# Optimization experiments

Measured on AMD Instinct MI355X. Metric: run time of the kernel, lower is better.

## Reference

```python
import jax, jax.numpy as jnp
import numpy as np
import math

B, H, W = 32, 512, 512
BS = 8
QUALITY = 50.0  # __scale_quality(75) = 200 - 2*75


def _make_dctmtx(bs=BS):
    m = np.empty((bs, bs), dtype=np.float32)
    for j in range(bs):
        for i in range(bs):
            if i == 0:
                m[i, j] = 1.0 / math.sqrt(bs)
            else:
                m[i, j] = math.sqrt(2.0 / bs) * math.cos(math.pi * (2 * j + 1) * i / (2 * bs))
    return jnp.asarray(m)


def _make_quantize():
    qY = np.array([[16,11,10,16,24,40,51,61],[12,12,14,19,26,58,60,55],
                   [14,13,16,24,40,57,69,56],[14,17,22,29,51,87,80,62],
                   [18,22,37,56,68,109,103,77],[24,35,55,64,81,104,113,92],
                   [49,64,78,87,103,121,120,101],[72,92,95,98,112,100,103,99]], dtype=np.float32) / 255.0
    qC = np.array([[17,18,24,47,99,99,99,99],[18,21,26,66,99,99,99,99],
                   [24,26,56,99,99,99,99,99],[47,66,99,99,99,99,99,99],
                   [99,99,99,99,99,99,99,99],[99,99,99,99,99,99,99,99],
                   [99,99,99,99,99,99,99,99],[99,99,99,99,99,99,99,99]], dtype=np.float32) / 255.0
    return jnp.asarray(np.stack([qY, qC, qC], axis=0))


def setup_inputs() -> dict:
    key = jax.random.key(0)
    x = jax.random.uniform(key, (B, 3, H, W), dtype=jnp.float32)
    return {"input": x, "quantize": _make_quantize(), "dctmtx": _make_dctmtx()}


def reference(input, quantize, dctmtx):
    bs = BS
    b, c, h, w = input.shape
    dt = input.dtype
    rgb = 255.0 * input
    # rgb -> ycbcr (3x3 color transform, offset cb/cr by 128, clamp)
    xf = jnp.array([[0.299, 0.587, 0.114],
                    [-0.168735892, -0.331264108, 0.5],
                    [0.5, -0.418687589, -0.081312411]], dtype=dt)
    off = jnp.array([0.0, 128.0, 128.0], dtype=dt)[None, :, None, None]
    ycbcr = jnp.clip(jnp.einsum('bchw,kc->bkhw', rgb, xf) + off, 0.0, 255.0)
    # 2x2 chroma subsample: replace Cb/Cr by 2x2 block means (Y untouched)
    yc = ycbcr[:, :1]
    cc = ycbcr[:, 1:].reshape(b, 2, h // 2, 2, w // 2, 2)
    cm = jnp.mean(cc, axis=(3, 5), keepdims=True)
    cc = jnp.broadcast_to(cm, cc.shape).reshape(b, 2, h, w)
    sample = jnp.concatenate([yc, cc], axis=1) - 128.0
    # extract 8x8 blocks -> [b, h/bs, w/bs, 3, bs, bs]
    blocks = sample.reshape(b, 3, h // bs, bs, w // bs, bs).transpose(0, 2, 4, 1, 3, 5)
    # 2D DCT: D @ X @ D^T
    dcts = jnp.einsum('ij,bhwcjk,lk->bhwcil', dctmtx, blocks, dctmtx)
    # quality-scaled quant table (broadcasts [3,8,8] over blocks)
    q = jnp.round(jnp.clip(jnp.round((jnp.round(quantize * 255.0) * QUALITY + 50.0) / 100.0), 1.0, 255.0))
    comp = jnp.round(dcts / q)
    decomp = jnp.round(comp * jax.lax.stop_gradient(q))
    # IDCT: D^T @ X @ D
    idcts = jnp.einsum('ji,bhwcjk,kl->bhwcil', dctmtx, decomp, dctmtx)
    # merge blocks back -> [b,3,h,w]
    ycbcr2 = idcts.transpose(0, 3, 1, 4, 2, 5).reshape(b, 3, h, w) + 128.0
    # ycbcr -> rgb
    xf2 = jnp.array([[1.0, 0.0, 1.402],
                     [1.0, -0.344136286, -0.714136286],
                     [1.0, 1.772, 0.0]], dtype=dt)
    im = ycbcr2 - off
    rgb2 = jnp.clip(jnp.einsum('bchw,kc->bkhw', im, xf2), 0.0, 255.0)
    return jnp.round(rgb2) / 255.0
```

## Files before the change

### kernel.cpp

```cpp
#include <hip/hip_runtime.h>

#define IN_H 512
#define IN_W 512


__device__ __forceinline__ float dpp_xor1(float x) {
    return __int_as_float(__builtin_amdgcn_mov_dpp(__float_as_int(x), 0xB1, 0xF, 0xF, true));
}
__device__ __forceinline__ float dpp_xor2(float x) {
    return __int_as_float(__builtin_amdgcn_mov_dpp(__float_as_int(x), 0x4E, 0xF, 0xF, true));
}
__device__ __forceinline__ float dpp_xor4(float x) {
    int i = __builtin_amdgcn_mov_dpp(__float_as_int(x), 0x141, 0xF, 0xF, true);
    i     = __builtin_amdgcn_mov_dpp(i,                 0x1B,  0xF, 0xF, true);
    return __int_as_float(i);
}

__global__ __launch_bounds__(256, 2) void jpeg_kernel(
    const float* __restrict__ in, const float* __restrict__ qz,
    const float* __restrict__ dmtx, float* __restrict__ out)
{
    __shared__ __align__(16) unsigned char smem[30464];
    double*  Ys  = (double*) (smem);
    double*  CbS = (double*) (smem + 17408);
    double*  CrS = (double*) (smem + 22016);
    double2* qt  = (double2*)(smem + 26624);
    double*  Dd  = (double*) (smem + 30080);
    float*   Dh  = (float*)  (smem + 30336);

    const int t   = threadIdx.x;
    const int blk = blockIdx.x;
    const int b   = blk >> 7;
    const int rr  = blk & 127;
    const int row0 = (rr >> 1) << 3;
    const int col0 = (rr & 1) << 8;
    const int chs = IN_H * IN_W;

    const int tile = t >> 3;
    const int h4   = (t >> 2) & 1;
    const int s    = t & 3;

    const int base = ((b * 3) * IN_H + row0 + 2 * s) * IN_W + col0 + tile * 8 + 4 * h4;
    float4 ra = *(const float4*)(in + base);
    float4 rb = *(const float4*)(in + base + IN_W);
    float4 ga = *(const float4*)(in + base + chs);
    float4 gb = *(const float4*)(in + base + chs + IN_W);
    float4 ba = *(const float4*)(in + base + 2 * chs);
    float4 bb = *(const float4*)(in + base + 2 * chs + IN_W);

    if (t < 192) {
        const int c = t >> 6, i = (t >> 3) & 7, l = t & 7;
        double v  = (double)qz[t];
        double t1 = rint((rint(v * 255.0) * 50.0 + 50.0) / 100.0);
        double q  = fmin(fmax(t1, 1.0), 255.0);
        qt[(c * 8 + l) * 9 + i] = make_double2(1.0 / q, q);
    }
    if (t < 32) {
        float dv = dmtx[(t >> 2) * 8 + (t & 3)];
        Dd[t] = (double)dv;
        Dh[t] = dv;
    }
    __syncthreads();

    {
        float rA[2][4] = {{ra.x,ra.y,ra.z,ra.w},{rb.x,rb.y,rb.z,rb.w}};
        float gA[2][4] = {{ga.x,ga.y,ga.z,ga.w},{gb.x,gb.y,gb.z,gb.w}};
        float bA[2][4] = {{ba.x,ba.y,ba.z,ba.w},{bb.x,bb.y,bb.z,bb.w}};

        double yv[2][4], cbv[2][4], crv[2][4];
        #pragma unroll
        for (int p = 0; p < 2; ++p) {
            #pragma unroll
            for (int k = 0; k < 4; ++k) {
                double R = 255.0 * (double)rA[p][k];
                double G = 255.0 * (double)gA[p][k];
                double B = 255.0 * (double)bA[p][k];
                double y  =  0.299*R + 0.587*G + 0.114*B;
                double cb = -0.168735892*R - 0.331264108*G + 0.5*B + 128.0;
                double cr =  0.5*R - 0.418687589*G - 0.081312411*B + 128.0;
                yv[p][k]  = fmin(fmax(y , 0.0), 255.0) - 128.0;
                cbv[p][k] = fmin(fmax(cb, 0.0), 255.0);
                crv[p][k] = fmin(fmax(cr, 0.0), 255.0);
            }
        }
        #pragma unroll
        for (int p = 0; p < 2; ++p) {
            double* yp = &Ys[tile * 68 + (2*s + p) * 8 + 4 * h4];
            *(double2*)(yp)     = make_double2(yv[p][0], yv[p][1]);
            *(double2*)(yp + 2) = make_double2(yv[p][2], yv[p][3]);
        }
        double m0 = (cbv[0][0]+cbv[0][1]+cbv[1][0]+cbv[1][1])*0.25 - 128.0;
        double m1 = (cbv[0][2]+cbv[0][3]+cbv[1][2]+cbv[1][3])*0.25 - 128.0;
        *(double2*)&CbS[tile * 18 + s * 4 + 2 * h4] = make_double2(m0, m1);
        double n0 = (crv[0][0]+crv[0][1]+crv[1][0]+crv[1][1])*0.25 - 128.0;
        double n1 = (crv[0][2]+crv[0][3]+crv[1][2]+crv[1][3])*0.25 - 128.0;
        *(double2*)&CrS[tile * 18 + s * 4 + 2 * h4] = make_double2(n0, n1);
    }
    __builtin_amdgcn_wave_barrier();

    const int q8 = t >> 3;
    const int l  = t & 7;
    double dl0, dl1, dl2, dl3;
    {
        double2 dA = *(const double2*)&Dd[l * 4];
        double2 dB = *(const double2*)&Dd[l * 4 + 2];
        dl0 = dA.x; dl1 = dA.y; dl2 = dB.x; dl3 = dB.y;
    }
    const double sgn  = (l & 1) ? -1.0 : 1.0;
    const double dl01 = dl0 + dl1, dl23 = dl2 + dl3;
    const bool sel1 = (l & 1) != 0;
    const bool sel2 = (l & 2) != 0;
    const bool sel4 = (l & 4) != 0;

    double e20[4], o20[4];
    {
        const double* basep = &Ys[q8 * 68];
        #pragma unroll
        for (int m = 0; m < 4; ++m) {
            double tp[2];
            #pragma unroll
            for (int hh = 0; hh < 2; ++hh) {
                const double* p = basep + (hh ? (7 - m) : m) * 8;
                double2 a0 = *(const double2*)(p);
                double2 a1 = *(const double2*)(p + 2);
                double2 a2 = *(const double2*)(p + 4);
                double2 a3 = *(const double2*)(p + 6);
                double v0 = fma(sgn, a3.y, a0.x);
                double v1 = fma(sgn, a3.x, a0.y);
                double v2 = fma(sgn, a2.y, a1.x);
                double v3 = fma(sgn, a2.x, a1.y);
                tp[hh] = dl0*v0 + dl1*v1 + dl2*v2 + dl3*v3;
            }
            e20[m] = tp[0] + tp[1];
            o20[m] = tp[0] - tp[1];
        }
    }
    double e21[4], o21[4], e22[4], o22[4];
    #pragma unroll
    for (int cc = 0; cc < 2; ++cc) {
        const double* basep = (cc == 0 ? CbS : CrS) + q8 * 18;
        double u4[4];
        #pragma unroll
        for (int j2 = 0; j2 < 4; ++j2) {
            double2 a0 = *(const double2*)(basep + j2 * 4);
            double2 a1 = *(const double2*)(basep + j2 * 4 + 2);
            u4[j2] = dl01 * fma(sgn, a1.y, a0.x) + dl23 * fma(sgn, a1.x, a0.y);
        }
        double ea = u4[0] + u4[3], oa = u4[0] - u4[3];
        double eb = u4[1] + u4[2], ob = u4[1] - u4[2];
        if (cc == 0) { e21[0]=e21[1]=ea; o21[0]=o21[1]=oa; e21[2]=e21[3]=eb; o21[2]=o21[3]=ob; }
        else         { e22[0]=e22[1]=ea; o22[0]=o22[1]=oa; e22[2]=e22[3]=eb; o22[2]=o22[3]=ob; }
    }

    float zo[3][8];
    {
        const double2* dd2 = (const double2*)Dd;
        #pragma unroll
        for (int i = 0; i < 8; ++i) {
            double2 dA = dd2[i * 2], dB = dd2[i * 2 + 1];
            #define ZQ(C, E, O) { \
                double a64 = (i & 1) \
                    ? dA.x*O[0] + dA.y*O[1] + dB.x*O[2] + dB.y*O[3] \
                    : dA.x*E[0] + dA.y*E[1] + dB.x*E[2] + dB.y*E[3]; \
                double2 qe = qt[(C * 8 + l) * 9 + i]; \
                zo[C][i] = (float)(rint(a64 * qe.x) * qe.y); }
            ZQ(0, e20, o20)
            ZQ(1, e21, o21)
            ZQ(2, e22, o22)
            #undef ZQ
        }
    }

    const float4* dh4p = (const float4*)Dh;
    float4 d0 = dh4p[0], d1 = dh4p[1], d2 = dh4p[2], d3 = dh4p[3];
    float4 d4 = dh4p[4], d5 = dh4p[5], d6 = dh4p[6], d7 = dh4p[7];

    float acc[3][8];

    #define BFLY(XF, SS, A, B) { float _t = (SS) ? (A) : (B); float _tx = XF(_t); \
                                 (A) = (SS) ? _tx : (A); (B) = (SS) ? (B) : _tx; }

    #define EPI(C) { \
        float se0 = zo[C][0]*d0.x + zo[C][2]*d2.x + zo[C][4]*d4.x + zo[C][6]*d6.x; \
        float se1 = zo[C][0]*d0.y + zo[C][2]*d2.y + zo[C][4]*d4.y + zo[C][6]*d6.y; \
        float se2 = zo[C][0]*d0.z + zo[C][2]*d2.z + zo[C][4]*d4.z + zo[C][6]*d6.z; \
        float se3 = zo[C][0]*d0.w + zo[C][2]*d2.w + zo[C][4]*d4.w + zo[C][6]*d6.w; \
        float so0 = zo[C][1]*d1.x + zo[C][3]*d3.x + zo[C][5]*d5.x + zo[C][7]*d7.x; \
        float so1 = zo[C][1]*d1.y + zo[C][3]*d3.y + zo[C][5]*d5.y + zo[C][7]*d7.y; \
        float so2 = zo[C][1]*d1.z + zo[C][3]*d3.z + zo[C][5]*d5.z + zo[C][7]*d7.z; \
        float so3 = zo[C][1]*d1.w + zo[C][3]*d3.w + zo[C][5]*d5.w + zo[C][7]*d7.w; \
        float u0 = se0+so0, u7 = se0-so0; \
        float u1 = se1+so1, u6 = se1-so1; \
        float u2 = se2+so2, u5 = se2-so2; \
        float u3 = se3+so3, u4v = se3-so3; \
         \
        BFLY(dpp_xor1, sel1, u0, u1)  BFLY(dpp_xor1, sel1, u2, u3) \
        BFLY(dpp_xor1, sel1, u4v, u5) BFLY(dpp_xor1, sel1, u6, u7) \
        BFLY(dpp_xor2, sel2, u0, u2)  BFLY(dpp_xor2, sel2, u1, u3) \
        BFLY(dpp_xor2, sel2, u4v, u6) BFLY(dpp_xor2, sel2, u5, u7) \
        BFLY(dpp_xor4, sel4, u0, u4v) BFLY(dpp_xor4, sel4, u1, u5) \
        BFLY(dpp_xor4, sel4, u2, u6)  BFLY(dpp_xor4, sel4, u3, u7) \
        float re0 = u0*d0.x + u2*d2.x + u4v*d4.x + u6*d6.x; \
        float re1 = u0*d0.y + u2*d2.y + u4v*d4.y + u6*d6.y; \
        float re2 = u0*d0.z + u2*d2.z + u4v*d4.z + u6*d6.z; \
        float re3 = u0*d0.w + u2*d2.w + u4v*d4.w + u6*d6.w; \
        float ro0 = u1*d1.x + u3*d3.x + u5*d5.x + u7*d7.x; \
        float ro1 = u1*d1.y + u3*d3.y + u5*d5.y + u7*d7.y; \
        float ro2 = u1*d1.z + u3*d3.z + u5*d5.z + u7*d7.z; \
        float ro3 = u1*d1.w + u3*d3.w + u5*d5.w + u7*d7.w; \
        acc[C][0]=re0+ro0; acc[C][7]=re0-ro0; \
        acc[C][1]=re1+ro1; acc[C][6]=re1-ro1; \
        acc[C][2]=re2+ro2; acc[C][5]=re2-ro2; \
        acc[C][3]=re3+ro3; acc[C][4]=re3-ro3; }

    EPI(0)
    EPI(1)
    EPI(2)
    #undef EPI
    #undef BFLY

    {
        const int obase = ((b * 3) * IN_H + row0 + l) * IN_W + col0 + q8 * 8;
        float R4[8], G4[8], B4[8];
        #pragma unroll
        for (int y = 0; y < 8; ++y) {
            float im0 = acc[0][y] + 128.0f;
            float im1 = acc[1][y];
            float im2 = acc[2][y];
            float R  = fminf(fmaxf(im0 + 1.402f*im2, 0.0f), 255.0f);
            float G  = fminf(fmaxf(im0 - 0.344136286f*im1 - 0.714136286f*im2, 0.0f), 255.0f);
            float Bv = fminf(fmaxf(im0 + 1.772f*im1, 0.0f), 255.0f);
            R4[y] = rintf(R)  * (1.0f/255.0f);
            G4[y] = rintf(G)  * (1.0f/255.0f);
            B4[y] = rintf(Bv) * (1.0f/255.0f);
        }
        *(float4*)(out + obase)               = make_float4(R4[0],R4[1],R4[2],R4[3]);
        *(float4*)(out + obase + 4)           = make_float4(R4[4],R4[5],R4[6],R4[7]);
        *(float4*)(out + obase + chs)         = make_float4(G4[0],G4[1],G4[2],G4[3]);
        *(float4*)(out + obase + chs + 4)     = make_float4(G4[4],G4[5],G4[6],G4[7]);
        *(float4*)(out + obase + 2*chs)       = make_float4(B4[0],B4[1],B4[2],B4[3]);
        *(float4*)(out + obase + 2*chs + 4)   = make_float4(B4[4],B4[5],B4[6],B4[7]);
    }
}

extern "C" void kernel_launch(void* const* d_in, const int* in_sizes, int n_in,
                              void* d_out, int out_size, void* d_ws, size_t ws_size,
                              hipStream_t stream) {
    (void)in_sizes; (void)n_in; (void)out_size; (void)d_ws; (void)ws_size;
    const float* in  = (const float*)d_in[0];
    const float* qz  = (const float*)d_in[1];
    const float* dm  = (const float*)d_in[2];
    float* out = (float*)d_out;
    dim3 grid(4096), blk(256);
    hipLaunchKernelGGL(jpeg_kernel, grid, blk, 0, stream, in, qz, dm, out);
}
```

Before: 182.2 us.

## Compute luma row DCT in registers via DPP exchanges instead of shared memory

```diff
diff --git a/kernel.cpp b/kernel.cpp
--- a/kernel.cpp
+++ b/kernel.cpp
@@ -16,17 +16,37 @@
     return __int_as_float(i);
 }
 
+__device__ __forceinline__ double dpp_xor1_d(double x) {
+    union { double d; int i[2]; } u; u.d = x;
+    u.i[0] = __builtin_amdgcn_mov_dpp(u.i[0], 0xB1, 0xF, 0xF, true);
+    u.i[1] = __builtin_amdgcn_mov_dpp(u.i[1], 0xB1, 0xF, 0xF, true);
+    return u.d;
+}
+__device__ __forceinline__ double dpp_xor2_d(double x) {
+    union { double d; int i[2]; } u; u.d = x;
+    u.i[0] = __builtin_amdgcn_mov_dpp(u.i[0], 0x4E, 0xF, 0xF, true);
+    u.i[1] = __builtin_amdgcn_mov_dpp(u.i[1], 0x4E, 0xF, 0xF, true);
+    return u.d;
+}
+__device__ __forceinline__ double dpp_xor4_d(double x) {
+    union { double d; int i[2]; } u; u.d = x;
+    u.i[0] = __builtin_amdgcn_mov_dpp(u.i[0], 0x141, 0xF, 0xF, true);
+    u.i[0] = __builtin_amdgcn_mov_dpp(u.i[0], 0x1B,  0xF, 0xF, true);
+    u.i[1] = __builtin_amdgcn_mov_dpp(u.i[1], 0x141, 0xF, 0xF, true);
+    u.i[1] = __builtin_amdgcn_mov_dpp(u.i[1], 0x1B,  0xF, 0xF, true);
+    return u.d;
+}
+
 __global__ __launch_bounds__(256, 2) void jpeg_kernel(
     const float* __restrict__ in, const float* __restrict__ qz,
     const float* __restrict__ dmtx, float* __restrict__ out)
 {
-    __shared__ __align__(16) unsigned char smem[30464];
-    double*  Ys  = (double*) (smem);
-    double*  CbS = (double*) (smem + 17408);
-    double*  CrS = (double*) (smem + 22016);
-    double2* qt  = (double2*)(smem + 26624);
-    double*  Dd  = (double*) (smem + 30080);
-    float*   Dh  = (float*)  (smem + 30336);
+    __shared__ __align__(16) unsigned char smem[13056];
+    double*  CbS = (double*) (smem);
+    double*  CrS = (double*) (smem + 4608);
+    double2* qt  = (double2*)(smem + 9216);
+    double*  Dd  = (double*) (smem + 12672);
+    float*   Dh  = (float*)  (smem + 12928);
 
     const int t   = threadIdx.x;
     const int blk = blockIdx.x;
@@ -62,12 +82,13 @@
     }
     __syncthreads();
 
+    double yv[2][4];
     {
         float rA[2][4] = {{ra.x,ra.y,ra.z,ra.w},{rb.x,rb.y,rb.z,rb.w}};
         float gA[2][4] = {{ga.x,ga.y,ga.z,ga.w},{gb.x,gb.y,gb.z,gb.w}};
         float bA[2][4] = {{ba.x,ba.y,ba.z,ba.w},{bb.x,bb.y,bb.z,bb.w}};
 
-        double yv[2][4], cbv[2][4], crv[2][4];
+        double cbv[2][4], crv[2][4];
         #pragma unroll
         for (int p = 0; p < 2; ++p) {
             #pragma unroll
@@ -83,12 +104,6 @@
                 crv[p][k] = fmin(fmax(cr, 0.0), 255.0);
             }
         }
-        #pragma unroll
-        for (int p = 0; p < 2; ++p) {
-            double* yp = &Ys[tile * 68 + (2*s + p) * 8 + 4 * h4];
-            *(double2*)(yp)     = make_double2(yv[p][0], yv[p][1]);
-            *(double2*)(yp + 2) = make_double2(yv[p][2], yv[p][3]);
-        }
         double m0 = (cbv[0][0]+cbv[0][1]+cbv[1][0]+cbv[1][1])*0.25 - 128.0;
         double m1 = (cbv[0][2]+cbv[0][3]+cbv[1][2]+cbv[1][3])*0.25 - 128.0;
         *(double2*)&CbS[tile * 18 + s * 4 + 2 * h4] = make_double2(m0, m1);
@@ -96,10 +111,56 @@
         double n1 = (crv[0][2]+crv[0][3]+crv[1][2]+crv[1][3])*0.25 - 128.0;
         *(double2*)&CrS[tile * 18 + s * 4 + 2 * h4] = make_double2(n0, n1);
     }
-    __builtin_amdgcn_wave_barrier();
 
     const int q8 = t >> 3;
     const int l  = t & 7;
+    const bool sel1 = (l & 1) != 0;
+    const bool sel2 = (l & 2) != 0;
+    const bool sel4 = (l & 4) != 0;
+    const bool hb   = (h4 != 0);
+
+    double e20[4], o20[4];
+    {
+        double recv[4];
+        #pragma unroll
+        for (int k = 0; k < 4; ++k) {
+            double x = hb ? yv[0][k] : yv[1][k];
+            recv[k] = dpp_xor4_d(x);
+        }
+        double ev[4], ov[4];
+        #pragma unroll
+        for (int j = 0; j < 4; ++j) {
+            double aj = hb ? recv[j]      : yv[0][j];
+            double bj = hb ? yv[1][3 - j] : recv[3 - j];
+            ev[j] = aj + bj;
+            ov[j] = aj - bj;
+        }
+        const float4* dh4 = (const float4*)Dh;
+        double G[8];
+        #pragma unroll
+        for (int i = 0; i < 8; ++i) {
+            float4 di = dh4[i];
+            const double* vv = (i & 1) ? ov : ev;
+            G[i] = (double)di.x*vv[0] + (double)di.y*vv[1]
+                 + (double)di.z*vv[2] + (double)di.w*vv[3];
+        }
+        #define BFLY64(XF, SS, A, B) { double _t = (SS) ? (A) : (B); double _tx = XF(_t); \
+                                       (A) = (SS) ? _tx : (A); (B) = (SS) ? (B) : _tx; }
+        BFLY64(dpp_xor1_d, sel1, G[0], G[1])  BFLY64(dpp_xor1_d, sel1, G[2], G[3])
+        BFLY64(dpp_xor1_d, sel1, G[4], G[5])  BFLY64(dpp_xor1_d, sel1, G[6], G[7])
+        BFLY64(dpp_xor2_d, sel2, G[0], G[2])  BFLY64(dpp_xor2_d, sel2, G[1], G[3])
+        BFLY64(dpp_xor2_d, sel2, G[4], G[6])  BFLY64(dpp_xor2_d, sel2, G[5], G[7])
+        BFLY64(dpp_xor4_d, sel4, G[0], G[4])  BFLY64(dpp_xor4_d, sel4, G[1], G[5])
+        BFLY64(dpp_xor4_d, sel4, G[2], G[6])  BFLY64(dpp_xor4_d, sel4, G[3], G[7])
+        #undef BFLY64
+        e20[0] = G[0] + G[7];  o20[0] = G[0] - G[7];
+        e20[1] = G[4] + G[3];  o20[1] = G[4] - G[3];
+        e20[2] = G[1] + G[6];  o20[2] = G[1] - G[6];
+        e20[3] = G[5] + G[2];  o20[3] = G[5] - G[2];
+    }
+
+    __builtin_amdgcn_wave_barrier();
+
     double dl0, dl1, dl2, dl3;
     {
         double2 dA = *(const double2*)&Dd[l * 4];
@@ -108,33 +169,7 @@
     }
     const double sgn  = (l & 1) ? -1.0 : 1.0;
     const double dl01 = dl0 + dl1, dl23 = dl2 + dl3;
-    const bool sel1 = (l & 1) != 0;
-    const bool sel2 = (l & 2) != 0;
-    const bool sel4 = (l & 4) != 0;
-
-    double e20[4], o20[4];
-    {
-        const double* basep = &Ys[q8 * 68];
-        #pragma unroll
-        for (int m = 0; m < 4; ++m) {
-            double tp[2];
-            #pragma unroll
-            for (int hh = 0; hh < 2; ++hh) {
-                const double* p = basep + (hh ? (7 - m) : m) * 8;
-                double2 a0 = *(const double2*)(p);
-                double2 a1 = *(const double2*)(p + 2);
-                double2 a2 = *(const double2*)(p + 4);
-                double2 a3 = *(const double2*)(p + 6);
-                double v0 = fma(sgn, a3.y, a0.x);
-                double v1 = fma(sgn, a3.x, a0.y);
-                double v2 = fma(sgn, a2.y, a1.x);
-                double v3 = fma(sgn, a2.x, a1.y);
-                tp[hh] = dl0*v0 + dl1*v1 + dl2*v2 + dl3*v3;
-            }
-            e20[m] = tp[0] + tp[1];
-            o20[m] = tp[0] - tp[1];
-        }
-    }
+
     double e21[4], o21[4], e22[4], o22[4];
     #pragma unroll
     for (int cc = 0; cc < 2; ++cc) {
```

New measurement: 181.4 us. About the same (-0.5%).
